# Kernel tuning notes

Measured on AMD Instinct MI355X. Metric: run time of the kernel, lower is better.

Reference implementation:

```python
import jax, jax.numpy as jnp
import numpy as np

N_NODES = 10000
N_EDGES = 160000
FEAT = 32
EMB = 32
VOCAB = 32000
EDGE_DIM = 9
HID = 32  # edge MLP hidden


def setup_inputs() -> dict:
    key = jax.random.key(0)
    ks = jax.random.split(key, 16)
    s = lambda *sh: 1.0 / np.sqrt(sh[0])
    inp = {
        "signal": jax.random.randint(ks[0], (1,), 0, VOCAB, dtype=jnp.int64) if jax.config.jax_enable_x64 else jax.random.randint(ks[0], (1,), 0, VOCAB).astype(jnp.int32),
        "x": jax.random.normal(ks[1], (N_NODES, FEAT), dtype=jnp.float32),
        "edge_index": jax.random.randint(ks[2], (2, N_EDGES), 0, N_NODES).astype(jnp.int32),
        "edge_attr": jax.random.normal(ks[3], (N_EDGES, EDGE_DIM), dtype=jnp.float32),
        # edge MLP 1: 9 -> 32 -> FEAT*EMB
        "w1a": jax.random.normal(ks[4], (EDGE_DIM, HID), dtype=jnp.float32) * s(EDGE_DIM),
        "b1a": jnp.zeros((HID,), jnp.float32),
        "w1b": jax.random.normal(ks[5], (HID, FEAT * EMB), dtype=jnp.float32) * s(HID),
        "b1b": jnp.zeros((FEAT * EMB,), jnp.float32),
        "root1": jax.random.normal(ks[6], (FEAT, EMB), dtype=jnp.float32) * s(FEAT),
        "bias1": jnp.zeros((EMB,), jnp.float32),
        # edge MLP 2: 9 -> 32 -> EMB*EMB
        "w2a": jax.random.normal(ks[7], (EDGE_DIM, HID), dtype=jnp.float32) * s(EDGE_DIM),
        "b2a": jnp.zeros((HID,), jnp.float32),
        "w2b": jax.random.normal(ks[8], (HID, EMB * EMB), dtype=jnp.float32) * s(HID),
        "b2b": jnp.zeros((EMB * EMB,), jnp.float32),
        "root2": jax.random.normal(ks[9], (EMB, EMB), dtype=jnp.float32) * s(EMB),
        "bias2": jnp.zeros((EMB,), jnp.float32),
        "emb_table": jax.random.normal(ks[10], (VOCAB, EMB), dtype=jnp.float32),
    }
    return inp


def nnconv(x, edge_index, edge_attr, wa, ba, wb, bb, root, bias, in_ch, out_ch):
    # edge MLP -> per-edge weight matrices [E, in_ch, out_ch]
    h = jax.nn.relu(edge_attr @ wa + ba)
    W_e = (h @ wb + bb).reshape(-1, in_ch, out_ch)
    src, dst = edge_index[0], edge_index[1]
    # gather source node features, per-edge matmul
    msg = jnp.einsum("ei,eio->eo", x[src], W_e)  # [E, out_ch]
    summed = jax.ops.segment_sum(msg, dst, num_segments=N_NODES)
    cnt = jax.ops.segment_sum(jnp.ones((msg.shape[0],), msg.dtype), dst, num_segments=N_NODES)
    aggr = summed / jnp.maximum(cnt, 1.0)[:, None]  # scatter-mean (0 for isolated nodes)
    return aggr + x @ root + bias


def reference(signal, x, edge_index, edge_attr,
              w1a, b1a, w1b, b1b, root1, bias1,
              w2a, b2a, w2b, b2b, root2, bias2, emb_table):
    h = jax.nn.relu(nnconv(x, edge_index, edge_attr, w1a, b1a, w1b, b1b, root1, bias1, FEAT, EMB))
    h = jax.nn.relu(nnconv(h, edge_index, edge_attr, w2a, b2a, w2b, b2b, root2, bias2, EMB, EMB))
    sig = emb_table[signal]          # [1, EMB]
    sig = sig[0]                      # squeeze leading 1 (matches torch branch)
    scores = h @ sig                  # [N]
    return jax.nn.log_softmax(scores, axis=0)
```

## Files before the change

kernel.cpp:

```cpp
#include <hip/hip_runtime.h>
#include <math.h>

#define NN 10000
#define NE 160000
#define C  32
#define ED 9
#define EAP 12

typedef __attribute__((ext_vector_type(8))) short short8v;
typedef __attribute__((ext_vector_type(4))) float float4v;

__device__ inline unsigned short f2bf(float f) {
    unsigned int u = __float_as_uint(f);
    return (unsigned short)((u + 0x7fffu + ((u >> 16) & 1u)) >> 16);
}

#define ZQ 10016
__global__ __launch_bounds__(256) void prep_kernel(uint4* __restrict__ zreg,
                                                   const float* __restrict__ w1b,
                                                   const float* __restrict__ w2b,
                                                   float* __restrict__ wbT1,
                                                   float* __restrict__ wbT2) {
    const int b = blockIdx.x, tid = threadIdx.x;
    if (b < 40) {
        const int i = b * 256 + tid;
        if (i < ZQ) zreg[i] = uint4{0u, 0u, 0u, 0u};
    } else if (b < 168) {
        const int idx = (b - 40) * 256 + tid;
        const int i = idx & 31, k = (idx >> 5) & 31, o = idx >> 10;
        wbT1[idx] = w1b[k * (C * C) + i * C + o];
    } else {
        const int idx = (b - 168) * 256 + tid;
        const int i = idx & 31, k = (idx >> 5) & 31, o = idx >> 10;
        wbT2[idx] = w2b[k * (C * C) + i * C + o];
    }
}

__global__ __launch_bounds__(256) void hist_kernel(const int* __restrict__ ei,
                                                   int* __restrict__ cnt_src,
                                                   int* __restrict__ cnt_dst) {
    const int e = blockIdx.x * 256 + threadIdx.x;
    if (e < NE) {
        atomicAdd(&cnt_src[ei[e]], 1);
        atomicAdd(&cnt_dst[ei[NE + e]], 1);
    }
}

__global__ __launch_bounds__(1024) void scan2_kernel(const int* __restrict__ cnt_src,
                                                     const int* __restrict__ cnt_dst,
                                                     int* __restrict__ offs,
                                                     int* __restrict__ doffs) {
    const int* cnt = blockIdx.x ? cnt_dst : cnt_src;
    int* out       = blockIdx.x ? doffs   : offs;
    __shared__ int wtot[16];
    const int t = threadIdx.x;
    const int lane = t & 63, wid = t >> 6;
    const int base = t * 10;
    int loc[10];
    int s = 0;
#pragma unroll
    for (int j = 0; j < 10; ++j) {
        int v = (base + j < NN) ? cnt[base + j] : 0;
        loc[j] = s;
        s += v;
    }
    int inc = s;
    for (int d = 1; d < 64; d <<= 1) {
        int v = __shfl_up(inc, d, 64);
        if (lane >= d) inc += v;
    }
    if (lane == 63) wtot[wid] = inc;
    __syncthreads();
    if (t < 16) {
        int w = wtot[t];
        for (int d = 1; d < 16; d <<= 1) {
            int v = __shfl_up(w, d, 64);
            if (t >= d) w += v;
        }
        wtot[t] = w;
    }
    __syncthreads();
    const int excl = inc - s + (wid ? wtot[wid - 1] : 0);
#pragma unroll
    for (int j = 0; j < 10; ++j)
        if (base + j < NN) out[base + j] = excl + loc[j];
    if (t == 1023) out[NN] = wtot[15];
}

__device__ __forceinline__ void u_body(int vb, int tid, float* __restrict__ xs,
                                       const float* __restrict__ xin,
                                       const float* __restrict__ wbT,
                                       const float* __restrict__ bb,
                                       unsigned short* __restrict__ UT,
                                       float* __restrict__ xb) {
    const int nb = (vb >> 2) * 16;
    const int o0 = (vb & 3) * 8;
    for (int t = tid; t < 16 * C; t += 256) xs[t] = xin[nb * C + t];
    __syncthreads();

    const int op = tid >> 5, k = tid & 31, o = o0 + op;
    float4v wv[8];
    const float* wp = wbT + ((size_t)o * C + k) * C;
#pragma unroll
    for (int i4 = 0; i4 < 8; ++i4)
        wv[i4] = *reinterpret_cast<const float4v*>(wp + i4 * 4);

#pragma unroll
    for (int n = 0; n < 16; ++n) {
        float acc = 0.f;
#pragma unroll
        for (int i4 = 0; i4 < 8; ++i4) {
            const float4v xv = *reinterpret_cast<const float4v*>(&xs[n * C + i4 * 4]);
            acc += xv.x * wv[i4].x + xv.y * wv[i4].y + xv.z * wv[i4].z + xv.w * wv[i4].w;
        }
        UT[(size_t)(nb + n) * (C * C) + o * C + k] = f2bf(acc);
    }
    if (o0 == 0) {
#pragma unroll
        for (int t = 0; t < 2; ++t) {
            const int idx = t * 256 + tid;
            const int n = idx >> 5, oo = idx & 31;
            float acc = 0.f;
#pragma unroll
            for (int i = 0; i < C; ++i) acc += xs[n * C + i] * bb[i * C + oo];
            xb[(size_t)(nb + n) * C + oo] = acc;
        }
    }
}

__global__ __launch_bounds__(256) void mid_kernel(const int* __restrict__ ei,
                                                  const float* __restrict__ ea,
                                                  const int* __restrict__ offs,
                                                  const int* __restrict__ doffs,
                                                  int* __restrict__ cur_src,
                                                  int* __restrict__ cur_dst,
                                                  int* __restrict__ pd,
                                                  float* __restrict__ ea_s,
                                                  const float* __restrict__ xin,
                                                  const float* __restrict__ wbT,
                                                  const float* __restrict__ bb,
                                                  unsigned short* __restrict__ UT,
                                                  float* __restrict__ xb) {
    __shared__ float xs[16 * C];
    const int b = blockIdx.x, tid = threadIdx.x;
    if (b < 625) {
        const int e = b * 256 + tid;
        if (e < NE) {
            const int sn  = ei[e];
            const int dn  = ei[NE + e];
            const int pos = offs[sn]  + atomicAdd(&cur_src[sn], 1);
            const int dpo = doffs[dn] + atomicAdd(&cur_dst[dn], 1);
            pd[pos] = dpo;
#pragma unroll
            for (int j = 0; j < ED; ++j)
                ea_s[(size_t)pos * EAP + j] = ea[(size_t)e * ED + j];
        }
    } else {
        u_body(b - 625, tid, xs, xin, wbT, bb, UT, xb);
    }
}

__global__ __launch_bounds__(256) void u_gemm2(const float* __restrict__ xin,
                                               const float* __restrict__ wbT,
                                               const float* __restrict__ bb,
                                               unsigned short* __restrict__ UT,
                                               float* __restrict__ xb) {
    __shared__ float xs[16 * C];
    u_body(blockIdx.x, threadIdx.x, xs, xin, wbT, bb, UT, xb);
}

__global__ __launch_bounds__(256) void edge5_kernel(const int* __restrict__ offs,
                                                    const int* __restrict__ pd,
                                                    const float* __restrict__ ea_s,
                                                    const float* __restrict__ wa,
                                                    const float* __restrict__ ba,
                                                    const unsigned short* __restrict__ UT,
                                                    const float* __restrict__ xb,
                                                    float* __restrict__ msg) {
    __shared__ float was[ED * C];
    __shared__ float bas[C];
    const int tid = threadIdx.x;
    for (int t = tid; t < ED * C; t += 256) was[t] = wa[t];
    if (tid < C) bas[tid] = ba[tid];
    __syncthreads();

    const int w  = tid >> 6;
    const int l  = tid & 63;
    const int s  = blockIdx.x * 4 + w;
    const int q  = l >> 4;
    const int el = l & 15;

    const int e0 = offs[s], e1 = offs[s + 1];
    if (e0 == e1) return;

    const unsigned short* up = UT + (size_t)s * (C * C);
    const short8v B1 = *reinterpret_cast<const short8v*>(up + el * C + q * 8);
    const short8v B2 = *reinterpret_cast<const short8v*>(up + (el + 16) * C + q * 8);
    const float c1 = xb[s * C + el];
    const float c2 = xb[s * C + el + 16];
    const float4v C1 = {c1, c1, c1, c1};
    const float4v C2 = {c2, c2, c2, c2};
    float hb[8];
#pragma unroll
    for (int i = 0; i < 8; ++i) hb[i] = bas[q * 8 + i];

    for (int pb = e0; pb < e1; pb += 16) {
        const int p  = pb + el;
        const int pc = (p < e1) ? p : e0;
        const float* eap = ea_s + (size_t)pc * EAP;
        const float4v ea0 = *reinterpret_cast<const float4v*>(eap);
        const float4v ea1 = *reinterpret_cast<const float4v*>(eap + 4);
        const float   ea8 = eap[8];

        float h[8];
#pragma unroll
        for (int i = 0; i < 8; ++i) h[i] = hb[i];
#pragma unroll
        for (int j = 0; j < ED; ++j) {
            const float ev = (j == 0) ? ea0.x : (j == 1) ? ea0.y : (j == 2) ? ea0.z
                           : (j == 3) ? ea0.w : (j == 4) ? ea1.x : (j == 5) ? ea1.y
                           : (j == 6) ? ea1.z : (j == 7) ? ea1.w : ea8;
            const float4v w0 = *reinterpret_cast<const float4v*>(&was[j * C + q * 8]);
            const float4v w1 = *reinterpret_cast<const float4v*>(&was[j * C + q * 8 + 4]);
            h[0] += ev * w0.x; h[1] += ev * w0.y; h[2] += ev * w0.z; h[3] += ev * w0.w;
            h[4] += ev * w1.x; h[5] += ev * w1.y; h[6] += ev * w1.z; h[7] += ev * w1.w;
        }
        union { int u[4]; short8v v; } A;
#pragma unroll
        for (int v = 0; v < 4; ++v) {
            const unsigned lo = f2bf(fmaxf(h[2 * v], 0.f));
            const unsigned hi = f2bf(fmaxf(h[2 * v + 1], 0.f));
            A.u[v] = (int)(lo | (hi << 16));
        }
        const float4v d1 = __builtin_amdgcn_mfma_f32_16x16x32_bf16(A.v, B1, C1, 0, 0, 0);
        const float4v d2 = __builtin_amdgcn_mfma_f32_16x16x32_bf16(A.v, B2, C2, 0, 0, 0);
#pragma unroll
        for (int r = 0; r < 4; ++r) {
            const int pe = pb + q * 4 + r;
            if (pe < e1) {
                const int mr = pd[pe];
                msg[(size_t)mr * C + el]      = d1[r];
                msg[(size_t)mr * C + el + 16] = d2[r];
            }
        }
    }
}

__global__ __launch_bounds__(256) void nodeagg1_kernel(const int* __restrict__ doffs,
                                                       const float* __restrict__ msg,
                                                       const float* __restrict__ xin,
                                                       const float* __restrict__ root,
                                                       const float* __restrict__ bias,
                                                       float* __restrict__ h1out) {
    __shared__ float rs[C * C];
    __shared__ float bs[C];
    __shared__ float xls[4][C];
    const int tid = threadIdx.x;
    for (int t = tid; t < C * C; t += 256) rs[t] = root[t];
    if (tid < C) bs[tid] = bias[tid];
    __syncthreads();

    const int w = tid >> 6, lane = tid & 63;
    const int half = lane >> 5, o = lane & 31;
    const int d = blockIdx.x * 4 + w;
    const int e0 = doffs[d], e1 = doffs[d + 1];

    float acc = 0.f;
    for (int p = e0 + half; p < e1; p += 2) acc += msg[(size_t)p * C + o];
    acc += __shfl_down(acc, 32, 64);
    if (lane < 32) xls[w][o] = xin[(size_t)d * C + o];
    if (lane < 32) {
        const float cn = fmaxf((float)(e1 - e0), 1.f);
        float a = bs[o] + acc / cn;
#pragma unroll
        for (int i = 0; i < C; ++i) a += xls[w][i] * rs[i * C + o];
        h1out[(size_t)d * C + o] = fmaxf(a, 0.f);
    }
}

__global__ __launch_bounds__(256) void nodeagg2_score(const int* __restrict__ doffs,
                                                      const float* __restrict__ msg,
                                                      const float* __restrict__ h1,
                                                      const float* __restrict__ root,
                                                      const float* __restrict__ bias,
                                                      const float* __restrict__ emb,
                                                      const int* __restrict__ signal,
                                                      float* __restrict__ scores) {
    __shared__ float rs[C * C];
    __shared__ float bs[C];
    __shared__ float sig[C];
    __shared__ float xls[4][C];
    const int tid = threadIdx.x;
    for (int t = tid; t < C * C; t += 256) rs[t] = root[t];
    if (tid < C) {
        bs[tid]  = bias[tid];
        sig[tid] = emb[(size_t)signal[0] * C + tid];
    }
    __syncthreads();

    const int w = tid >> 6, lane = tid & 63;
    const int half = lane >> 5, o = lane & 31;
    const int d = blockIdx.x * 4 + w;
    const int e0 = doffs[d], e1 = doffs[d + 1];

    float acc = 0.f;
    for (int p = e0 + half; p < e1; p += 2) acc += msg[(size_t)p * C + o];
    acc += __shfl_down(acc, 32, 64);
    if (lane < 32) xls[w][o] = h1[(size_t)d * C + o];
    if (lane < 32) {
        const float cn = fmaxf((float)(e1 - e0), 1.f);
        float a = bs[o] + acc / cn;
#pragma unroll
        for (int i = 0; i < C; ++i) a += xls[w][i] * rs[i * C + o];
        float val = fmaxf(a, 0.f) * sig[o];
#pragma unroll
        for (int off = 16; off; off >>= 1) val += __shfl_xor(val, off, 32);
        if (o == 0) scores[d] = val;
    }
}

__global__ __launch_bounds__(1024) void reduce_out_kernel(const float* __restrict__ scores,
                                                          float* __restrict__ out) {
    __shared__ float sm[16];
    __shared__ float ss[16];
    const int tid = threadIdx.x;
    float m = -INFINITY;
    for (int n = tid; n < NN; n += 1024) m = fmaxf(m, scores[n]);
    for (int off = 32; off; off >>= 1) m = fmaxf(m, __shfl_down(m, off, 64));
    if ((tid & 63) == 0) sm[tid >> 6] = m;
    __syncthreads();
    if (tid == 0) {
        float mm = sm[0];
        for (int w = 1; w < 16; ++w) mm = fmaxf(mm, sm[w]);
        sm[0] = mm;
    }
    __syncthreads();
    const float gmax = sm[0];
    float s = 0.f;
    for (int n = tid; n < NN; n += 1024) s += expf(scores[n] - gmax);
    for (int off = 32; off; off >>= 1) s += __shfl_down(s, off, 64);
    if ((tid & 63) == 0) ss[tid >> 6] = s;
    __syncthreads();
    if (tid == 0) {
        float t = 0.f;
        for (int w = 0; w < 16; ++w) t += ss[w];
        ss[0] = logf(t);
    }
    __syncthreads();
    const float sub = gmax + ss[0];
    for (int n = tid; n < NN; n += 1024) out[n] = scores[n] - sub;
}

extern "C" void kernel_launch(void* const* d_in, const int* in_sizes, int n_in,
                              void* d_out, int out_size, void* d_ws, size_t ws_size,
                              hipStream_t stream) {
    const int*   signal = (const int*)d_in[0];
    const float* x      = (const float*)d_in[1];
    const int*   ei     = (const int*)d_in[2];
    const float* ea     = (const float*)d_in[3];
    const float* w1a    = (const float*)d_in[4];
    const float* b1a    = (const float*)d_in[5];
    const float* w1b    = (const float*)d_in[6];
    const float* b1b    = (const float*)d_in[7];
    const float* root1  = (const float*)d_in[8];
    const float* bias1  = (const float*)d_in[9];
    const float* w2a    = (const float*)d_in[10];
    const float* b2a    = (const float*)d_in[11];
    const float* w2b    = (const float*)d_in[12];
    const float* b2b    = (const float*)d_in[13];
    const float* root2  = (const float*)d_in[14];
    const float* bias2  = (const float*)d_in[15];
    const float* emb    = (const float*)d_in[16];

    float* ws = (float*)d_ws;
    unsigned short* UT = (unsigned short*)ws;
    float* msg     = ws + 5120000;
    float* xb      = msg + 5120000;
    float* h1      = xb + 320000;
    float* ea_s    = h1 + 320000;
    float* wbT1    = ea_s + 1920000;
    float* wbT2    = wbT1 + 32768;
    float* scores  = wbT2 + 32768;
    int*   offs    = (int*)(scores + 10000);
    int*   doffs   = offs + 10016;
    int*   pd      = doffs + 10016;
    int*   cnt_src = pd + 160000;
    int*   cnt_dst = cnt_src + NN;
    int*   cur_src = cnt_dst + NN;
    int*   cur_dst = cur_src + NN;

    prep_kernel<<<296, 256, 0, stream>>>((uint4*)cnt_src, w1b, w2b, wbT1, wbT2);
    hist_kernel<<<(NE + 255) / 256, 256, 0, stream>>>(ei, cnt_src, cnt_dst);
    scan2_kernel<<<2, 1024, 0, stream>>>(cnt_src, cnt_dst, offs, doffs);
    mid_kernel<<<3125, 256, 0, stream>>>(ei, ea, offs, doffs, cur_src, cur_dst,
                                         pd, ea_s, x, wbT1, b1b, UT, xb);
    edge5_kernel<<<2500, 256, 0, stream>>>(offs, pd, ea_s, w1a, b1a, UT, xb, msg);
    nodeagg1_kernel<<<2500, 256, 0, stream>>>(doffs, msg, x, root1, bias1, h1);
    u_gemm2<<<2500, 256, 0, stream>>>(h1, wbT2, b2b, UT, xb);
    edge5_kernel<<<2500, 256, 0, stream>>>(offs, pd, ea_s, w2a, b2a, UT, xb, msg);
    nodeagg2_score<<<2500, 256, 0, stream>>>(doffs, msg, h1, root2, bias2,
                                             emb, signal, scores);
    reduce_out_kernel<<<1, 1024, 0, stream>>>(scores, (float*)d_out);
}
```

Before: 157.1 us.

## Compute per-node U projection with bf16 MFMA using hi/lo split

Replaces the scalar FP32 per-node projection of node features through the edge-MLP second-layer weights with MFMA 16x16x32 bf16 instructions. Weights are pre-converted to bf16 in a transposed layout, and node features are split into high and low bf16 parts to keep near-FP32 accuracy. Each block now handles 16 nodes across all 1024 outputs, so the grid shrinks four-fold. This cuts ALU work in the U GEMMs. The cost is a second MFMA per tile and bf16 rounding of the weights.

```diff
diff --git a/kernel.cpp b/kernel.cpp
--- a/kernel.cpp
+++ b/kernel.cpp
@@ -14,25 +14,26 @@
     unsigned int u = __float_as_uint(f);
     return (unsigned short)((u + 0x7fffu + ((u >> 16) & 1u)) >> 16);
 }
+__device__ inline float bf2f(unsigned int us) { return __uint_as_float(us << 16); }
 
 #define ZQ 10016
 __global__ __launch_bounds__(256) void prep_kernel(uint4* __restrict__ zreg,
                                                    const float* __restrict__ w1b,
                                                    const float* __restrict__ w2b,
-                                                   float* __restrict__ wbT1,
-                                                   float* __restrict__ wbT2) {
+                                                   unsigned short* __restrict__ wbB1,
+                                                   unsigned short* __restrict__ wbB2) {
     const int b = blockIdx.x, tid = threadIdx.x;
     if (b < 40) {
         const int i = b * 256 + tid;
         if (i < ZQ) zreg[i] = uint4{0u, 0u, 0u, 0u};
     } else if (b < 168) {
         const int idx = (b - 40) * 256 + tid;
-        const int i = idx & 31, k = (idx >> 5) & 31, o = idx >> 10;
-        wbT1[idx] = w1b[k * (C * C) + i * C + o];
+        const int i = idx & 31, j = idx >> 5;
+        wbB1[idx] = f2bf(w1b[(j & 31) * (C * C) + i * C + (j >> 5)]);
     } else {
         const int idx = (b - 168) * 256 + tid;
-        const int i = idx & 31, k = (idx >> 5) & 31, o = idx >> 10;
-        wbT2[idx] = w2b[k * (C * C) + i * C + o];
+        const int i = idx & 31, j = idx >> 5;
+        wbB2[idx] = f2bf(w2b[(j & 31) * (C * C) + i * C + (j >> 5)]);
     }
 }
 
@@ -87,44 +88,58 @@
     if (t == 1023) out[NN] = wtot[15];
 }
 
-__device__ __forceinline__ void u_body(int vb, int tid, float* __restrict__ xs,
-                                       const float* __restrict__ xin,
-                                       const float* __restrict__ wbT,
-                                       const float* __restrict__ bb,
-                                       unsigned short* __restrict__ UT,
-                                       float* __restrict__ xb) {
-    const int nb = (vb >> 2) * 16;
-    const int o0 = (vb & 3) * 8;
-    for (int t = tid; t < 16 * C; t += 256) xs[t] = xin[nb * C + t];
-    __syncthreads();
-
-    const int op = tid >> 5, k = tid & 31, o = o0 + op;
-    float4v wv[8];
-    const float* wp = wbT + ((size_t)o * C + k) * C;
-#pragma unroll
-    for (int i4 = 0; i4 < 8; ++i4)
-        wv[i4] = *reinterpret_cast<const float4v*>(wp + i4 * 4);
-
-#pragma unroll
-    for (int n = 0; n < 16; ++n) {
+__device__ __forceinline__ void u_mfma_body(int vb, int tid,
+                                            float* __restrict__ xs,
+                                            unsigned int* __restrict__ bhi,
+                                            unsigned int* __restrict__ blo,
+                                            const float* __restrict__ xin,
+                                            const unsigned short* __restrict__ wbB,
+                                            const float* __restrict__ bb,
+                                            unsigned short* __restrict__ UT,
+                                            float* __restrict__ xb) {
+    const int nb = vb * 16;
+    {
+        const float2 v = *reinterpret_cast<const float2*>(xin + nb * C + 2 * tid);
+        xs[2 * tid] = v.x; xs[2 * tid + 1] = v.y;
+        const unsigned hx = f2bf(v.x), hy = f2bf(v.y);
+        bhi[tid] = hx | (hy << 16);
+        const float lx = v.x - bf2f(hx), ly = v.y - bf2f(hy);
+        blo[tid] = (unsigned)f2bf(lx) | ((unsigned)f2bf(ly) << 16);
+    }
+    __syncthreads();
+
+    const int w = tid >> 6, l = tid & 63;
+    const int r15 = l & 15, q = l >> 4;
+    const short8v Bh = *reinterpret_cast<const short8v*>(
+        reinterpret_cast<const unsigned short*>(bhi) + r15 * C + q * 8);
+    const short8v Bl = *reinterpret_cast<const short8v*>(
+        reinterpret_cast<const unsigned short*>(blo) + r15 * C + q * 8);
+    const float4v Z = {0.f, 0.f, 0.f, 0.f};
+
+#pragma unroll
+    for (int cg = 0; cg < 4; ++cg) {
+        const int jbase = w * 256 + cg * 64 + 0;
+#pragma unroll
+        for (int t4 = 0; t4 < 4; ++t4) {
+            const int jb = jbase + t4 * 16;
+            const short8v A = *reinterpret_cast<const short8v*>(
+                wbB + (size_t)(jb + r15) * C + q * 8);
+            float4v acc = __builtin_amdgcn_mfma_f32_16x16x32_bf16(A, Bl, Z, 0, 0, 0);
+            acc = __builtin_amdgcn_mfma_f32_16x16x32_bf16(A, Bh, acc, 0, 0, 0);
+            ushort4 pk;
+            pk.x = f2bf(acc[0]); pk.y = f2bf(acc[1]);
+            pk.z = f2bf(acc[2]); pk.w = f2bf(acc[3]);
+            *reinterpret_cast<ushort4*>(UT + (size_t)(nb + r15) * (C * C) + jb + q * 4) = pk;
+        }
+    }
+#pragma unroll
+    for (int t = 0; t < 2; ++t) {
+        const int idx = t * 256 + tid;
+        const int n = idx >> 5, oo = idx & 31;
         float acc = 0.f;
 #pragma unroll
-        for (int i4 = 0; i4 < 8; ++i4) {
-            const float4v xv = *reinterpret_cast<const float4v*>(&xs[n * C + i4 * 4]);
-            acc += xv.x * wv[i4].x + xv.y * wv[i4].y + xv.z * wv[i4].z + xv.w * wv[i4].w;
-        }
-        UT[(size_t)(nb + n) * (C * C) + o * C + k] = f2bf(acc);
-    }
-    if (o0 == 0) {
-#pragma unroll
-        for (int t = 0; t < 2; ++t) {
-            const int idx = t * 256 + tid;
-            const int n = idx >> 5, oo = idx & 31;
-            float acc = 0.f;
-#pragma unroll
-            for (int i = 0; i < C; ++i) acc += xs[n * C + i] * bb[i * C + oo];
-            xb[(size_t)(nb + n) * C + oo] = acc;
-        }
+        for (int i = 0; i < C; ++i) acc += xs[n * C + i] * bb[i * C + oo];
+        xb[(size_t)(nb + n) * C + oo] = acc;
     }
 }
 
@@ -137,11 +152,12 @@
                                                   int* __restrict__ pd,
                                                   float* __restrict__ ea_s,
                                                   const float* __restrict__ xin,
-                                                  const float* __restrict__ wbT,
+                                                  const unsigned short* __restrict__ wbB,
                                                   const float* __restrict__ bb,
                                                   unsigned short* __restrict__ UT,
                                                   float* __restrict__ xb) {
     __shared__ float xs[16 * C];
+    __shared__ unsigned int bhi[256], blo[256];
     const int b = blockIdx.x, tid = threadIdx.x;
     if (b < 625) {
         const int e = b * 256 + tid;
@@ -156,17 +172,18 @@
                 ea_s[(size_t)pos * EAP + j] = ea[(size_t)e * ED + j];
         }
     } else {
-        u_body(b - 625, tid, xs, xin, wbT, bb, UT, xb);
-    }
-}
-
-__global__ __launch_bounds__(256) void u_gemm2(const float* __restrict__ xin,
-                                               const float* __restrict__ wbT,
-                                               const float* __restrict__ bb,
-                                               unsigned short* __restrict__ UT,
-                                               float* __restrict__ xb) {
+        u_mfma_body(b - 625, tid, xs, bhi, blo, xin, wbB, bb, UT, xb);
+    }
+}
+
+__global__ __launch_bounds__(256) void u_mfma(const float* __restrict__ xin,
+                                              const unsigned short* __restrict__ wbB,
+                                              const float* __restrict__ bb,
+                                              unsigned short* __restrict__ UT,
+                                              float* __restrict__ xb) {
     __shared__ float xs[16 * C];
-    u_body(blockIdx.x, threadIdx.x, xs, xin, wbT, bb, UT, xb);
+    __shared__ unsigned int bhi[256], blo[256];
+    u_mfma_body(blockIdx.x, threadIdx.x, xs, bhi, blo, xin, wbB, bb, UT, xb);
 }
 
 __global__ __launch_bounds__(256) void edge5_kernel(const int* __restrict__ offs,
@@ -378,9 +395,9 @@
     float* xb      = msg + 5120000;
     float* h1      = xb + 320000;
     float* ea_s    = h1 + 320000;
-    float* wbT1    = ea_s + 1920000;
-    float* wbT2    = wbT1 + 32768;
-    float* scores  = wbT2 + 32768;
+    unsigned short* wbB1 = (unsigned short*)(ea_s + 1920000);
+    unsigned short* wbB2 = wbB1 + 32768;
+    float* scores  = ea_s + 1920000 + 32768;
     int*   offs    = (int*)(scores + 10000);
     int*   doffs   = offs + 10016;
     int*   pd      = doffs + 10016;
@@ -389,14 +406,14 @@
     int*   cur_src = cnt_dst + NN;
     int*   cur_dst = cur_src + NN;
 
-    prep_kernel<<<296, 256, 0, stream>>>((uint4*)cnt_src, w1b, w2b, wbT1, wbT2);
+    prep_kernel<<<296, 256, 0, stream>>>((uint4*)cnt_src, w1b, w2b, wbB1, wbB2);
     hist_kernel<<<(NE + 255) / 256, 256, 0, stream>>>(ei, cnt_src, cnt_dst);
     scan2_kernel<<<2, 1024, 0, stream>>>(cnt_src, cnt_dst, offs, doffs);
-    mid_kernel<<<3125, 256, 0, stream>>>(ei, ea, offs, doffs, cur_src, cur_dst,
-                                         pd, ea_s, x, wbT1, b1b, UT, xb);
+    mid_kernel<<<1250, 256, 0, stream>>>(ei, ea, offs, doffs, cur_src, cur_dst,
+                                         pd, ea_s, x, wbB1, b1b, UT, xb);
     edge5_kernel<<<2500, 256, 0, stream>>>(offs, pd, ea_s, w1a, b1a, UT, xb, msg);
     nodeagg1_kernel<<<2500, 256, 0, stream>>>(doffs, msg, x, root1, bias1, h1);
-    u_gemm2<<<2500, 256, 0, stream>>>(h1, wbT2, b2b, UT, xb);
+    u_mfma<<<625, 256, 0, stream>>>(h1, wbB2, b2b, UT, xb);
     edge5_kernel<<<2500, 256, 0, stream>>>(offs, pd, ea_s, w2a, b2a, UT, xb, msg);
     nodeagg2_score<<<2500, 256, 0, stream>>>(doffs, msg, h1, root2, bias2,
                                              emb, signal, scores);
```

Result: faster. 143.8 us (-8.4%).
